# Kernel optimization log

Hardware: AMD Instinct MI355X
Metric: run time of the kernel (lower is better)

## Reference

```python
import jax, jax.numpy as jnp
import numpy as np

B, F, H, K, E = 512, 1280, 2560, 8, 9  # batch, feat_dim, 2*feat_dim, branching, n_internal
# Tree: root=node 0 (expert 0); level-1 nodes 1..8 (experts 1..8); level-2 leaves 9..72.

def setup_inputs() -> dict:
    key = jax.random.key(0)
    k0, k1, k2, k3, k4 = jax.random.split(key, 5)
    x = jax.random.normal(k0, (B, F), dtype=jnp.float32)
    W1 = jax.random.normal(k1, (E, F, H), dtype=jnp.float32) / np.sqrt(F)
    b1 = jnp.zeros((E, H), dtype=jnp.float32)
    W2 = jax.random.normal(k2, (E, H, K), dtype=jnp.float32) / np.sqrt(H)
    b2 = jnp.zeros((E, K), dtype=jnp.float32)
    return {"x": x, "W1": W1, "b1": b1, "W2": W2, "b2": b2}

def reference(x, W1, b1, W2, b2):
    # Batched experts: Linear(F->H) -> ReLU -> Linear(H->K), softmax over children.
    h = jax.nn.relu(jnp.einsum('bf,efh->ebh', x, W1) + b1[:, None, :])  # [E,B,H]
    logits = jnp.einsum('ebh,ehk->ebk', h, W2) + b2[:, None, :]          # [E,B,K]
    probs = jax.nn.softmax(logits, axis=-1)                              # [E,B,K]
    # Path products root->node for every node (matches leaf_probs in torch code).
    p0 = jnp.ones((1, x.shape[0]), dtype=x.dtype)        # root: prob 1        [1,B]
    p1 = probs[0].T                                       # nodes 1..8          [K,B]
    # leaves 9..72: parent of node n is 1+(n-9)//K, child index (n-9)%K
    p2 = (p1[:, None, :] * jnp.transpose(probs[1:E], (0, 2, 1))).reshape(K * K, -1)  # [64,B]
    leaf_probs = jnp.concatenate([p0, p1, p2], axis=0).T  # [B, 73]
    return leaf_probs, logits
```

## Files before the change

### kernel.cpp

```cpp
#include <hip/hip_runtime.h>

#define TB 512
#define TF 1280
#define TH 2560
#define TK 8
#define TE 9

typedef unsigned short ushortT;
typedef unsigned long long u64;
typedef __attribute__((ext_vector_type(8))) short short8;
typedef __attribute__((ext_vector_type(4))) short short4v;
typedef __attribute__((ext_vector_type(4))) float floatx4;

__device__ __forceinline__ unsigned short f2bf(float f) {
  union { float f; unsigned u; } v; v.f = f;
  unsigned r = v.u + 0x7fffu + ((v.u >> 16) & 1u);
  return (unsigned short)(r >> 16);
}

__device__ __forceinline__ unsigned pk2(float a, float b) {
  union { float f; unsigned u; } ua, ub; ua.f = a; ub.f = b;
  unsigned ra = ua.u + 0x7fffu + ((ua.u >> 16) & 1u);
  unsigned rb = ub.u + 0x7fffu + ((ub.u >> 16) & 1u);
  return __builtin_amdgcn_perm(rb, ra, 0x07060302);
}

__device__ __forceinline__ void gl_lds16(const void* g, void* l) {
  __builtin_amdgcn_global_load_lds(
      (const __attribute__((address_space(1))) unsigned*)g,
      (__attribute__((address_space(3))) unsigned*)l, 16, 0, 0);
}

__global__ __launch_bounds__(256) void prep_all(
    const float* __restrict__ x, const float* __restrict__ W1,
    const float* __restrict__ W2,
    u64* __restrict__ xq, ushortT* __restrict__ W2t, u64* __restrict__ W1p) {
  const int b = blockIdx.x;
  const int t = threadIdx.x;
  if (b < 7200) {
    const int nt = b % 10;
    const int kt = (b / 10) % 80;
    const int e  = b / 800;
    const int tk = t >> 6, tc = t & 63;
    const int k0 = kt * 16 + tk * 4;
    const int n0 = nt * 256 + tc * 4;
    const float* src = W1 + ((long)e * TF + k0) * TH + n0;
    floatx4 v0 = *(const floatx4*)(src);
    floatx4 v1 = *(const floatx4*)(src + TH);
    floatx4 v2 = *(const floatx4*)(src + 2 * TH);
    floatx4 v3 = *(const floatx4*)(src + 3 * TH);
    u64 q[4];
#pragma unroll
    for (int i = 0; i < 4; ++i)
      q[i] = (u64)pk2(v0[i], v1[i]) | ((u64)pk2(v2[i], v3[i]) << 32);
    u64* dst = W1p + ((long)(e * 320 + (k0 >> 2)) * TH + n0);
    *(ulonglong2*)(dst)     = make_ulonglong2(q[0], q[1]);
    *(ulonglong2*)(dst + 2) = make_ulonglong2(q[2], q[3]);
  } else {
    const int i = (b - 7200) * 256 + t;
    if (i < 320 * 512) {
      const int kq = i >> 9, m = i & 511;
      floatx4 v = *(const floatx4*)(x + (long)m * TF + kq * 4);
      xq[i] = (u64)pk2(v.x, v.y) | ((u64)pk2(v.z, v.w) << 32);
    } else {
      const int o = i - 320 * 512;
      if (o < TE * TK * TH) {
        const int hcol = o % TH;
        const int rest = o / TH;
        const int n = rest & 7;
        const int e = rest >> 3;
        W2t[(long)(e * TK + n) * TH + hcol] = f2bf(W2[((long)e * TH + hcol) * TK + n]);
      }
    }
  }
}

__global__ __launch_bounds__(256) void prepass(
    const float* __restrict__ x, const float* __restrict__ W2,
    u64* __restrict__ xq, ushortT* __restrict__ W2t) {
  const int i = blockIdx.x * 256 + threadIdx.x;
  if (i < 320 * 512) {
    const int kq = i >> 9, m = i & 511;
    floatx4 v = *(const floatx4*)(x + (long)m * TF + kq * 4);
    xq[i] = (u64)pk2(v.x, v.y) | ((u64)pk2(v.z, v.w) << 32);
  } else {
    const int o = i - 320 * 512;
    if (o < TE * TK * TH) {
      const int hcol = o % TH;
      const int rest = o / TH;
      const int n = rest & 7;
      const int e = rest >> 3;
      W2t[(long)(e * TK + n) * TH + hcol] = f2bf(W2[((long)e * TH + hcol) * TK + n]);
    }
  }
}

__global__ __launch_bounds__(256) void gemm1_relu(
    const u64* __restrict__ xq, const u64* __restrict__ W1p,
    const float* __restrict__ b1, ushortT* __restrict__ h) {
  __shared__ __align__(16) u64 Aq[8 * 132];
  __shared__ __align__(16) u64 Bq[8 * 132];
  const int t = threadIdx.x;
  const int lane = t & 63, w = t >> 6;
  const int bid0 = blockIdx.x;
  const int bid = (bid0 & 7) * 90 + (bid0 >> 3);
  const int mt = bid & 3;
  const int ctile = bid >> 2;
  const int e = ctile / 20;
  const int hbase = (ctile % 20) * 128;
  const int m0 = mt * 128;
  const int wm = w & 1, wn = w >> 1;
  const int lm = lane & 15, lq = lane >> 4;

  const u64* agB = xq + m0 + lane * 2;
  const u64* bgB = W1p + ((long)e * 320) * TH + hbase + lane * 2;

  floatx4 acc[4][4];
#pragma unroll
  for (int i = 0; i < 4; ++i)
#pragma unroll
    for (int j = 0; j < 4; ++j) acc[i][j] = (floatx4){0.f, 0.f, 0.f, 0.f};

  for (int kt = 0; kt < 40; ++kt) {
    const int r0 = kt * 8;
    gl_lds16(agB + (long)(r0 + w) * 512, &Aq[w * 132]);
    gl_lds16(agB + (long)(r0 + w + 4) * 512, &Aq[(w + 4) * 132]);
    gl_lds16(bgB + (long)(r0 + w) * TH, &Bq[w * 132]);
    gl_lds16(bgB + (long)(r0 + w + 4) * TH, &Bq[(w + 4) * 132]);
    __syncthreads();

    short8 af[4], bf[4];
#pragma unroll
    for (int mg = 0; mg < 4; ++mg) {
      const int m = wm * 64 + mg * 16 + lm;
      ((u64*)&af[mg])[0] = Aq[(2 * lq) * 132 + m];
      ((u64*)&af[mg])[1] = Aq[(2 * lq + 1) * 132 + m];
    }
#pragma unroll
    for (int ng = 0; ng < 4; ++ng) {
      const int n = wn * 64 + ng * 16 + lm;
      ((u64*)&bf[ng])[0] = Bq[(2 * lq) * 132 + n];
      ((u64*)&bf[ng])[1] = Bq[(2 * lq + 1) * 132 + n];
    }
#pragma unroll
    for (int mg = 0; mg < 4; ++mg)
#pragma unroll
      for (int ng = 0; ng < 4; ++ng)
        acc[mg][ng] = __builtin_amdgcn_mfma_f32_16x16x32_bf16(af[mg], bf[ng], acc[mg][ng], 0, 0, 0);
    __syncthreads();
  }

#pragma unroll
  for (int mg = 0; mg < 4; ++mg) {
    const int row = m0 + wm * 64 + mg * 16 + lq * 4;
#pragma unroll
    for (int ng = 0; ng < 4; ++ng) {
      const int col = hbase + wn * 64 + ng * 16 + lm;
      const float bias = b1[e * TH + col];
      floatx4 c = acc[mg][ng];
#pragma unroll
      for (int r = 0; r < 4; ++r) {
        float v = c[r] + bias;
        v = v > 0.f ? v : 0.f;
        h[((long)e * TB + row + r) * TH + col] = f2bf(v);
      }
    }
  }
}

__global__ __launch_bounds__(256) void gemm1_fb(
    const float* __restrict__ x, const float* __restrict__ W1,
    const float* __restrict__ b1, ushortT* __restrict__ h) {
  __shared__ __align__(16) ushortT As[128 * 40];
  __shared__ __align__(16) ushortT Bs[128 * 40];
  const int t = threadIdx.x;
  const int tileN = blockIdx.x;
  const int e = tileN / 20;
  const int hbase = (tileN % 20) * 128;
  const int m0 = blockIdx.y * 128;
  const int lane = t & 63, w = t >> 6;
  const int wm = w & 1, wn = w >> 1;
  const int lm = lane & 15, lq = lane >> 4;
  const int lk = lq * 8;
  floatx4 acc[4][4];
#pragma unroll
  for (int i = 0; i < 4; ++i)
#pragma unroll
    for (int j = 0; j < 4; ++j) acc[i][j] = (floatx4){0.f, 0.f, 0.f, 0.f};
  const float* wp = W1 + (long)e * TF * TH + hbase;
  const int cA = (t & 7) * 4;
  const int mA = t >> 3;
  const int nB = t & 127;
  const int gB = t >> 7;
  for (int kt = 0; kt < TF / 32; ++kt) {
    const int k0 = kt * 32;
    if (kt) __syncthreads();
#pragma unroll
    for (int i = 0; i < 4; ++i) {
      const int m = mA + 32 * i;
      floatx4 v = *(const floatx4*)(x + (long)(m0 + m) * TF + k0 + cA);
      short4v s; s.x = f2bf(v.x); s.y = f2bf(v.y); s.z = f2bf(v.z); s.w = f2bf(v.w);
      *(short4v*)&As[m * 40 + cA] = s;
    }
    {
      const float* bp = wp + (long)k0 * TH + nB;
#pragma unroll
      for (int q = 0; q < 4; ++q) {
        const int k4 = gB * 16 + q * 4;
        float f0 = bp[(long)(k4 + 0) * TH];
        float f1 = bp[(long)(k4 + 1) * TH];
        float f2 = bp[(long)(k4 + 2) * TH];
        float f3 = bp[(long)(k4 + 3) * TH];
        short4v s; s.x = f2bf(f0); s.y = f2bf(f1); s.z = f2bf(f2); s.w = f2bf(f3);
        *(short4v*)&Bs[nB * 40 + k4] = s;
      }
    }
    __syncthreads();
    short8 af[4], bfr[4];
#pragma unroll
    for (int mg = 0; mg < 4; ++mg)
      af[mg] = *(const short8*)&As[(wm * 64 + mg * 16 + lm) * 40 + lk];
#pragma unroll
    for (int ng = 0; ng < 4; ++ng)
      bfr[ng] = *(const short8*)&Bs[(wn * 64 + ng * 16 + lm) * 40 + lk];
#pragma unroll
    for (int mg = 0; mg < 4; ++mg)
#pragma unroll
      for (int ng = 0; ng < 4; ++ng)
        acc[mg][ng] = __builtin_amdgcn_mfma_f32_16x16x32_bf16(af[mg], bfr[ng], acc[mg][ng], 0, 0, 0);
  }
#pragma unroll
  for (int mg = 0; mg < 4; ++mg) {
    const int row = m0 + wm * 64 + mg * 16 + lq * 4;
#pragma unroll
    for (int ng = 0; ng < 4; ++ng) {
      const int col = hbase + wn * 64 + ng * 16 + lm;
      const float bias = b1[e * TH + col];
      floatx4 c = acc[mg][ng];
#pragma unroll
      for (int r = 0; r < 4; ++r) {
        float v = c[r] + bias;
        v = v > 0.f ? v : 0.f;
        h[((long)e * TB + row + r) * TH + col] = f2bf(v);
      }
    }
  }
}

__global__ __launch_bounds__(512) void gemm2_softmax(
    const ushortT* __restrict__ h, const ushortT* __restrict__ W2t,
    const float* __restrict__ b2, float* __restrict__ logits_out,
    float* __restrict__ probs) {
  __shared__ float Ls[8][16][8];
  const int t = threadIdx.x;
  const int lane = t & 63, w = t >> 6;
  const int e = blockIdx.x >> 5;
  const int r0 = (blockIdx.x & 31) * 16;
  const int lm = lane & 15, lq = lane >> 4;

  const ushortT* hp = h + ((long)(e * TB + r0 + lm)) * TH + w * 320 + lq * 8;
  const int bn = lm < 8 ? lm : 7;
  const ushortT* wp = W2t + ((long)(e * TK + bn)) * TH + w * 320 + lq * 8;

  floatx4 acc = (floatx4){0.f, 0.f, 0.f, 0.f};
#pragma unroll
  for (int kt = 0; kt < 10; ++kt) {
    short8 a = *(const short8*)(hp + kt * 32);
    short8 b = *(const short8*)(wp + kt * 32);
    acc = __builtin_amdgcn_mfma_f32_16x16x32_bf16(a, b, acc, 0, 0, 0);
  }
  if (lm < 8) {
#pragma unroll
    for (int r = 0; r < 4; ++r) Ls[w][lq * 4 + r][lm] = acc[r];
  }
  __syncthreads();
  if (w == 0 && lm < 8) {
    const float bias = b2[e * TK + lm];
#pragma unroll
    for (int r = 0; r < 4; ++r) {
      const int row = lq * 4 + r;
      float v = Ls[0][row][lm] + Ls[1][row][lm] + Ls[2][row][lm] + Ls[3][row][lm]
              + Ls[4][row][lm] + Ls[5][row][lm] + Ls[6][row][lm] + Ls[7][row][lm]
              + bias;
      float mx = v;
      mx = fmaxf(mx, __shfl_xor(mx, 1, 64));
      mx = fmaxf(mx, __shfl_xor(mx, 2, 64));
      mx = fmaxf(mx, __shfl_xor(mx, 4, 64));
      float ex = __expf(v - mx);
      float sm = ex;
      sm += __shfl_xor(sm, 1, 64);
      sm += __shfl_xor(sm, 2, 64);
      sm += __shfl_xor(sm, 4, 64);
      const long idx = ((long)e * TB + r0 + row) * TK + lm;
      logits_out[idx] = v;
      probs[idx] = ex / sm;
    }
  }
}

__global__ __launch_bounds__(256) void leafk(const float* __restrict__ probs,
                                             float* __restrict__ out) {
  const int idx = blockIdx.x * 256 + threadIdx.x;
  if (idx >= TB * 73) return;
  const int b = idx / 73, c = idx % 73;
  float v;
  if (c == 0) {
    v = 1.0f;
  } else if (c < 9) {
    v = probs[(long)b * TK + (c - 1)];
  } else {
    const int i = (c - 9) >> 3, j = (c - 9) & 7;
    v = probs[(long)b * TK + i] * probs[((long)(1 + i) * TB + b) * TK + j];
  }
  out[idx] = v;
}

extern "C" void kernel_launch(void* const* d_in, const int* in_sizes, int n_in,
                              void* d_out, int out_size, void* d_ws, size_t ws_size,
                              hipStream_t stream) {
  const float* x  = (const float*)d_in[0];
  const float* W1 = (const float*)d_in[1];
  const float* b1 = (const float*)d_in[2];
  const float* W2 = (const float*)d_in[3];
  const float* b2 = (const float*)d_in[4];
  float* out = (float*)d_out;

  ushortT* h     = (ushortT*)d_ws;
  float*   probs = (float*)((char*)d_ws + 23592960);
  u64*     xq    = (u64*)((char*)d_ws + 23740416);
  ushortT* W2t   = (ushortT*)((char*)d_ws + 25051136);
  u64*     W1p   = (u64*)((char*)d_ws + 25419776);
  const size_t NEED = 25419776 + 58982400;
  float* logits_out = out + TB * 73;

  if (ws_size >= NEED) {
    prep_all<<<8560, 256, 0, stream>>>(x, W1, W2, xq, W2t, W1p);
    gemm1_relu<<<720, 256, 0, stream>>>(xq, W1p, b1, h);
  } else {
    prepass<<<1360, 256, 0, stream>>>(x, W2, xq, W2t);
    gemm1_fb<<<dim3(180, 4), 256, 0, stream>>>(x, W1, b1, h);
  }
  gemm2_softmax<<<TE * 32, 512, 0, stream>>>(h, W2t, b2, logits_out, probs);
  leafk<<<(TB * 73 + 255) / 256, 256, 0, stream>>>(probs, out);
}
```

Measured before the change: 232.1 us.

## Replace GEMM1 with 256x256-tile 8-wave ping-pong pipelined kernel and swizzled packing

The prep kernel now packs W1 and x into 16KB per-tile slots, transposed to K-contiguous bf16 with an XOR swizzle that avoids LDS bank conflicts. GEMM1 is replaced by a 512-thread kernel with 256x256 output tiles and a double-buffered 128KB LDS. Global-to-LDS loads are interleaved with MFMA phases using barriers, waitcnt and setprio. The aim is more data reuse per tile and better overlap of loads with compute. The cost is only 180 blocks, which underfills the 256 CUs, plus a large LDS footprint.

```diff
diff --git a/kernel.cpp b/kernel.cpp
--- a/kernel.cpp
+++ b/kernel.cpp
@@ -5,6 +5,8 @@
 #define TH 2560
 #define TK 8
 #define TE 9
+#define SLOT 16384
+#define BUFSZ 65536
 
 typedef unsigned short ushortT;
 typedef unsigned long long u64;
@@ -31,46 +33,62 @@
       (__attribute__((address_space(3))) unsigned*)l, 16, 0, 0);
 }
 
+__device__ __forceinline__ int swz(int o) { return o ^ (((o >> 7) & 7) << 4); }
+
 __global__ __launch_bounds__(256) void prep_all(
     const float* __restrict__ x, const float* __restrict__ W1,
     const float* __restrict__ W2,
-    u64* __restrict__ xq, ushortT* __restrict__ W2t, u64* __restrict__ W1p) {
+    char* __restrict__ Apk, ushortT* __restrict__ W2t, char* __restrict__ W1p) {
   const int b = blockIdx.x;
   const int t = threadIdx.x;
-  if (b < 7200) {
-    const int nt = b % 10;
-    const int kt = (b / 10) % 80;
-    const int e  = b / 800;
-    const int tk = t >> 6, tc = t & 63;
-    const int k0 = kt * 16 + tk * 4;
-    const int n0 = nt * 256 + tc * 4;
-    const float* src = W1 + ((long)e * TF + k0) * TH + n0;
+  if (b < 3600) {
+    __shared__ ushortT Ts[256 * 40];
+    const int khalf = b & 1;
+    const int kt = (b >> 1) % 20;
+    const int nt = ((b >> 1) / 20) % 10;
+    const int e = b / 400;
+    const int kbase = kt * 64 + khalf * 32;
+    const int nbase = nt * 256;
+    const int kr = t >> 6, n4 = (t & 63) * 4;
+#pragma unroll
+    for (int kk = 0; kk < 8; ++kk) {
+      const int k2 = kk * 4 + kr;
+      floatx4 v = *(const floatx4*)(W1 + ((long)e * TF + kbase + k2) * TH + nbase + n4);
+#pragma unroll
+      for (int i = 0; i < 4; ++i) Ts[(n4 + i) * 40 + k2] = f2bf(v[i]);
+    }
+    __syncthreads();
+    char* dstbase = W1p + (long)b * SLOT;
+#pragma unroll
+    for (int p = 0; p < 4; ++p) {
+      const int op = (p * 256 + t) * 16;
+      const int o = swz(op);
+      const int r = o >> 6, k2c = (o & 63) >> 1;
+      short8 v = *(const short8*)&Ts[r * 40 + k2c];
+      *(short8*)(dstbase + op) = v;
+    }
+  } else if (b < 3920) {
+    const int i = (b - 3600) * 256 + t;
+    const int cc = i & 1023, slot = i >> 10;
+    const int khalf = slot & 1, s2 = slot >> 1;
+    const int kt = s2 % 20, mt = s2 / 20;
+    const int op = cc * 16;
+    const int o = swz(op);
+    const int r = o >> 6, k2 = (o & 63) >> 1;
+    const float* src = x + (long)(mt * 256 + r) * TF + kt * 64 + khalf * 32 + k2;
     floatx4 v0 = *(const floatx4*)(src);
-    floatx4 v1 = *(const floatx4*)(src + TH);
-    floatx4 v2 = *(const floatx4*)(src + 2 * TH);
-    floatx4 v3 = *(const floatx4*)(src + 3 * TH);
-    u64 q[4];
-#pragma unroll
-    for (int i = 0; i < 4; ++i)
-      q[i] = (u64)pk2(v0[i], v1[i]) | ((u64)pk2(v2[i], v3[i]) << 32);
-    u64* dst = W1p + ((long)(e * 320 + (k0 >> 2)) * TH + n0);
-    *(ulonglong2*)(dst)     = make_ulonglong2(q[0], q[1]);
-    *(ulonglong2*)(dst + 2) = make_ulonglong2(q[2], q[3]);
+    floatx4 v1 = *(const floatx4*)(src + 4);
+    u64 q0 = (u64)pk2(v0.x, v0.y) | ((u64)pk2(v0.z, v0.w) << 32);
+    u64 q1 = (u64)pk2(v1.x, v1.y) | ((u64)pk2(v1.z, v1.w) << 32);
+    *(ulonglong2*)(Apk + (long)i * 16) = make_ulonglong2(q0, q1);
   } else {
-    const int i = (b - 7200) * 256 + t;
-    if (i < 320 * 512) {
-      const int kq = i >> 9, m = i & 511;
-      floatx4 v = *(const floatx4*)(x + (long)m * TF + kq * 4);
-      xq[i] = (u64)pk2(v.x, v.y) | ((u64)pk2(v.z, v.w) << 32);
-    } else {
-      const int o = i - 320 * 512;
-      if (o < TE * TK * TH) {
-        const int hcol = o % TH;
-        const int rest = o / TH;
-        const int n = rest & 7;
-        const int e = rest >> 3;
-        W2t[(long)(e * TK + n) * TH + hcol] = f2bf(W2[((long)e * TH + hcol) * TK + n]);
-      }
+    const int o = (b - 3920) * 256 + t;
+    if (o < TE * TK * TH) {
+      const int hcol = o % TH;
+      const int rest = o / TH;
+      const int n = rest & 7;
+      const int e = rest >> 3;
+      W2t[(long)(e * TK + n) * TH + hcol] = f2bf(W2[((long)e * TH + hcol) * TK + n]);
     }
   }
 }
@@ -95,69 +113,129 @@
   }
 }
 
-__global__ __launch_bounds__(256) void gemm1_relu(
-    const u64* __restrict__ xq, const u64* __restrict__ W1p,
+__global__ __launch_bounds__(512, 2) void gemm1_8p(
+    const char* __restrict__ Apk, const char* __restrict__ Bpk,
     const float* __restrict__ b1, ushortT* __restrict__ h) {
-  __shared__ __align__(16) u64 Aq[8 * 132];
-  __shared__ __align__(16) u64 Bq[8 * 132];
+  __shared__ __align__(16) char lds[131072];
   const int t = threadIdx.x;
   const int lane = t & 63, w = t >> 6;
-  const int bid0 = blockIdx.x;
-  const int bid = (bid0 & 7) * 90 + (bid0 >> 3);
-  const int mt = bid & 3;
-  const int ctile = bid >> 2;
-  const int e = ctile / 20;
-  const int hbase = (ctile % 20) * 128;
-  const int m0 = mt * 128;
-  const int wm = w & 1, wn = w >> 1;
+  const int wm = w >> 2, wn = w & 3;
   const int lm = lane & 15, lq = lane >> 4;
-
-  const u64* agB = xq + m0 + lane * 2;
-  const u64* bgB = W1p + ((long)e * 320) * TH + hbase + lane * 2;
-
-  floatx4 acc[4][4];
-#pragma unroll
-  for (int i = 0; i < 4; ++i)
+  const int bid = blockIdx.x;
+  const int e = bid / 20;
+  const int rem = bid % 20;
+  const int nt = rem >> 1, mt = rem & 1;
+
+  const char* Ab = Apk + (long)(mt * 20) * 2 * SLOT;
+  const char* Bb = Bpk + (long)((e * 10 + nt) * 20) * 2 * SLOT;
+
+  int oA[8], oB[4];
+#pragma unroll
+  for (int mi = 0; mi < 8; ++mi)
+    oA[mi] = swz((wm * 128 + mi * 16 + lm) * 64 + lq * 16);
+#pragma unroll
+  for (int ni = 0; ni < 4; ++ni)
+    oB[ni] = swz((wn * 64 + ni * 16 + lm) * 64 + lq * 16);
+
+  auto STAGE = [&](int tile, int half) {
+    if (tile >= 20) return;
+    const char* src = (half & 1)
+        ? Bb + (long)(tile * 2 + (half >> 1)) * SLOT
+        : Ab + (long)(tile * 2 + (half >> 1)) * SLOT;
+    char* dst = lds + (tile & 1) * BUFSZ + half * SLOT + w * 1024;
+    gl_lds16(src + t * 16, dst);
+    gl_lds16(src + 8192 + t * 16, dst + 8192);
+  };
+
+  floatx4 acc[8][4];
+#pragma unroll
+  for (int i = 0; i < 8; ++i)
 #pragma unroll
     for (int j = 0; j < 4; ++j) acc[i][j] = (floatx4){0.f, 0.f, 0.f, 0.f};
 
-  for (int kt = 0; kt < 40; ++kt) {
-    const int r0 = kt * 8;
-    gl_lds16(agB + (long)(r0 + w) * 512, &Aq[w * 132]);
-    gl_lds16(agB + (long)(r0 + w + 4) * 512, &Aq[(w + 4) * 132]);
-    gl_lds16(bgB + (long)(r0 + w) * TH, &Bq[w * 132]);
-    gl_lds16(bgB + (long)(r0 + w + 4) * TH, &Bq[(w + 4) * 132]);
-    __syncthreads();
-
-    short8 af[4], bf[4];
-#pragma unroll
-    for (int mg = 0; mg < 4; ++mg) {
-      const int m = wm * 64 + mg * 16 + lm;
-      ((u64*)&af[mg])[0] = Aq[(2 * lq) * 132 + m];
-      ((u64*)&af[mg])[1] = Aq[(2 * lq + 1) * 132 + m];
-    }
-#pragma unroll
-    for (int ng = 0; ng < 4; ++ng) {
-      const int n = wn * 64 + ng * 16 + lm;
-      ((u64*)&bf[ng])[0] = Bq[(2 * lq) * 132 + n];
-      ((u64*)&bf[ng])[1] = Bq[(2 * lq + 1) * 132 + n];
-    }
-#pragma unroll
-    for (int mg = 0; mg < 4; ++mg)
-#pragma unroll
-      for (int ng = 0; ng < 4; ++ng)
-        acc[mg][ng] = __builtin_amdgcn_mfma_f32_16x16x32_bf16(af[mg], bf[ng], acc[mg][ng], 0, 0, 0);
-    __syncthreads();
-  }
-
-#pragma unroll
-  for (int mg = 0; mg < 4; ++mg) {
-    const int row = m0 + wm * 64 + mg * 16 + lq * 4;
-#pragma unroll
-    for (int ng = 0; ng < 4; ++ng) {
-      const int col = hbase + wn * 64 + ng * 16 + lm;
+  STAGE(0, 0); STAGE(0, 1); STAGE(0, 2); STAGE(0, 3);
+  STAGE(1, 0); STAGE(1, 1); STAGE(1, 2);
+  asm volatile("s_waitcnt vmcnt(6)" ::: "memory");
+  __builtin_amdgcn_s_barrier();
+
+  for (int j = 0; j < 20; ++j) {
+    const char* buf = lds + (j & 1) * BUFSZ;
+    short8 af[8], bfA, bfB;
+#pragma unroll
+    for (int mi = 0; mi < 8; ++mi)
+      af[mi] = *(const short8*)(buf + 0 * SLOT + oA[mi]);
+    bfA = *(const short8*)(buf + 1 * SLOT + oB[0]);
+    bfB = *(const short8*)(buf + 1 * SLOT + oB[1]);
+    STAGE(j + 1, 3);
+    __builtin_amdgcn_s_barrier();
+    asm volatile("s_waitcnt lgkmcnt(0)" ::: "memory");
+    __builtin_amdgcn_sched_barrier(0);
+    __builtin_amdgcn_s_setprio(1);
+#pragma unroll
+    for (int mi = 0; mi < 8; ++mi) {
+      acc[mi][0] = __builtin_amdgcn_mfma_f32_16x16x32_bf16(af[mi], bfA, acc[mi][0], 0, 0, 0);
+      acc[mi][1] = __builtin_amdgcn_mfma_f32_16x16x32_bf16(af[mi], bfB, acc[mi][1], 0, 0, 0);
+    }
+    __builtin_amdgcn_s_setprio(0);
+    __builtin_amdgcn_s_barrier();
+    bfA = *(const short8*)(buf + 1 * SLOT + oB[2]);
+    bfB = *(const short8*)(buf + 1 * SLOT + oB[3]);
+    STAGE(j + 2, 0);
+    __builtin_amdgcn_s_barrier();
+    asm volatile("s_waitcnt lgkmcnt(0)" ::: "memory");
+    __builtin_amdgcn_sched_barrier(0);
+    __builtin_amdgcn_s_setprio(1);
+#pragma unroll
+    for (int mi = 0; mi < 8; ++mi) {
+      acc[mi][2] = __builtin_amdgcn_mfma_f32_16x16x32_bf16(af[mi], bfA, acc[mi][2], 0, 0, 0);
+      acc[mi][3] = __builtin_amdgcn_mfma_f32_16x16x32_bf16(af[mi], bfB, acc[mi][3], 0, 0, 0);
+    }
+    __builtin_amdgcn_s_setprio(0);
+    __builtin_amdgcn_s_barrier();
+#pragma unroll
+    for (int mi = 0; mi < 8; ++mi)
+      af[mi] = *(const short8*)(buf + 2 * SLOT + oA[mi]);
+    bfA = *(const short8*)(buf + 3 * SLOT + oB[0]);
+    bfB = *(const short8*)(buf + 3 * SLOT + oB[1]);
+    STAGE(j + 2, 1);
+    __builtin_amdgcn_s_barrier();
+    asm volatile("s_waitcnt lgkmcnt(0)" ::: "memory");
+    __builtin_amdgcn_sched_barrier(0);
+    __builtin_amdgcn_s_setprio(1);
+#pragma unroll
+    for (int mi = 0; mi < 8; ++mi) {
+      acc[mi][0] = __builtin_amdgcn_mfma_f32_16x16x32_bf16(af[mi], bfA, acc[mi][0], 0, 0, 0);
+      acc[mi][1] = __builtin_amdgcn_mfma_f32_16x16x32_bf16(af[mi], bfB, acc[mi][1], 0, 0, 0);
+    }
+    __builtin_amdgcn_s_setprio(0);
+    __builtin_amdgcn_s_barrier();
+    bfA = *(const short8*)(buf + 3 * SLOT + oB[2]);
+    bfB = *(const short8*)(buf + 3 * SLOT + oB[3]);
+    STAGE(j + 2, 2);
+    asm volatile("s_waitcnt vmcnt(6)" ::: "memory");
+    __builtin_amdgcn_s_barrier();
+    asm volatile("s_waitcnt lgkmcnt(0)" ::: "memory");
+    __builtin_amdgcn_sched_barrier(0);
+    __builtin_amdgcn_s_setprio(1);
+#pragma unroll
+    for (int mi = 0; mi < 8; ++mi) {
+      acc[mi][2] = __builtin_amdgcn_mfma_f32_16x16x32_bf16(af[mi], bfA, acc[mi][2], 0, 0, 0);
+      acc[mi][3] = __builtin_amdgcn_mfma_f32_16x16x32_bf16(af[mi], bfB, acc[mi][3], 0, 0, 0);
+    }
+    __builtin_amdgcn_s_setprio(0);
+    __builtin_amdgcn_s_barrier();
+  }
+
+  const int rowbase = mt * 256 + wm * 128 + lq * 4;
+  const int colbase = nt * 256 + wn * 64 + lm;
+#pragma unroll
+  for (int mi = 0; mi < 8; ++mi) {
+    const int row = rowbase + mi * 16;
+#pragma unroll
+    for (int ni = 0; ni < 4; ++ni) {
+      const int col = colbase + ni * 16;
       const float bias = b1[e * TH + col];
-      floatx4 c = acc[mg][ng];
+      floatx4 c = acc[mi][ni];
 #pragma unroll
       for (int r = 0; r < 4; ++r) {
         float v = c[r] + bias;
@@ -327,17 +405,17 @@
 
   ushortT* h     = (ushortT*)d_ws;
   float*   probs = (float*)((char*)d_ws + 23592960);
-  u64*     xq    = (u64*)((char*)d_ws + 23740416);
+  char*    Apk   = (char*)d_ws + 23740416;
   ushortT* W2t   = (ushortT*)((char*)d_ws + 25051136);
-  u64*     W1p   = (u64*)((char*)d_ws + 25419776);
+  char*    W1p   = (char*)d_ws + 25419776;
   const size_t NEED = 25419776 + 58982400;
   float* logits_out = out + TB * 73;
 
   if (ws_size >= NEED) {
-    prep_all<<<8560, 256, 0, stream>>>(x, W1, W2, xq, W2t, W1p);
-    gemm1_relu<<<720, 256, 0, stream>>>(xq, W1p, b1, h);
+    prep_all<<<4640, 256, 0, stream>>>(x, W1, W2, Apk, W2t, W1p);
+    gemm1_8p<<<180, 512, 0, stream>>>(Apk, W1p, b1, h);
   } else {
-    prepass<<<1360, 256, 0, stream>>>(x, W2, xq, W2t);
+    prepass<<<1360, 256, 0, stream>>>(x, W2, (u64*)Apk, W2t);
     gemm1_fb<<<dim3(180, 4), 256, 0, stream>>>(x, W1, b1, h);
   }
   gemm2_softmax<<<TE * 32, 512, 0, stream>>>(h, W2t, b2, logits_out, probs);
```

Result: no change. 235.6 us (+1.5%).
